# Optimization experiments

Hardware: AMD Instinct MI355X
Metric: run time of the kernel (lower is better)

The kernel has to match this reference:

```python
import jax, jax.numpy as jnp
import numpy as np

N, E, D, H, G = 50000, 1_600_000, 13, 32, 128
EPS = 1e-5


def _lin(k, fan_in, fan_out):
    kw, kb = jax.random.split(k)
    bound = 1.0 / np.sqrt(fan_in)
    W = jax.random.uniform(kw, (fan_in, fan_out), jnp.float32, -bound, bound)
    b = jax.random.uniform(kb, (fan_out,), jnp.float32, -bound, bound)
    return W, b


def setup_inputs() -> dict:
    key = jax.random.key(0)
    ks = jax.random.split(key, 10)
    x = jax.random.normal(ks[0], (N, D), jnp.float32)
    edge_index = jax.random.randint(ks[1], (2, E), 0, N)
    batch = jnp.sort(jax.random.randint(ks[2], (N,), 0, G))
    bn_gamma = jnp.ones((D,), jnp.float32)
    bn_beta = jnp.zeros((D,), jnp.float32)
    in_w1, in_b1 = _lin(ks[3], D, H)
    in_w2, in_b2 = _lin(ks[4], H, H)
    conv_w1, conv_b1 = _lin(ks[5], 2 * (H + D), 2 * H)
    conv_w2, conv_b2 = _lin(ks[6], 2 * H, H)
    out_w1, out_b1 = _lin(ks[7], H + D, H)
    out_w2, out_b2 = _lin(ks[8], H, 1)
    return dict(x=x, edge_index=edge_index, batch=batch,
                bn_gamma=bn_gamma, bn_beta=bn_beta,
                in_w1=in_w1, in_b1=in_b1, in_w2=in_w2, in_b2=in_b2,
                conv_w1=conv_w1, conv_b1=conv_b1, conv_w2=conv_w2, conv_b2=conv_b2,
                out_w1=out_w1, out_b1=out_b1, out_w2=out_w2, out_b2=out_b2)


def reference(x, edge_index, batch, bn_gamma, bn_beta,
              in_w1, in_b1, in_w2, in_b2,
              conv_w1, conv_b1, conv_w2, conv_b2,
              out_w1, out_b1, out_w2, out_b2):
    # BatchNorm1d (training-mode batch statistics, biased variance)
    mu = jnp.mean(x, axis=0)
    var = jnp.mean((x - mu) ** 2, axis=0)
    X = (x - mu) / jnp.sqrt(var + EPS) * bn_gamma + bn_beta  # [N, D]
    # inputnet
    Hn = jnp.tanh(jax.nn.relu(X @ in_w1 + in_b1) @ in_w2 + in_b2)  # [N, H]
    feat = jnp.concatenate([Hn, X], axis=-1)  # [N, H+D]
    # n_iters = 1 EdgeConv iteration: message = nn([x_i, x_j - x_i]), aggr='add' at target i
    src, dst = edge_index[0], edge_index[1]
    x_i = feat[dst]                               # [E, H+D] target
    x_j = feat[src]                               # [E, H+D] source
    m = jnp.concatenate([x_i, x_j - x_i], axis=-1)  # [E, 2(H+D)]
    m = jnp.tanh(jax.nn.relu(m @ conv_w1 + conv_b1) @ conv_w2 + conv_b2)  # [E, H]
    Hn = jax.ops.segment_sum(m, dst, num_segments=N)  # [N, H]
    feat = jnp.concatenate([Hn, X], axis=-1)  # [N, H+D]
    # global_mean_pool over graphs
    sums = jax.ops.segment_sum(feat, batch, num_segments=G)  # [G, H+D]
    counts = jax.ops.segment_sum(jnp.ones((feat.shape[0], 1), feat.dtype), batch, num_segments=G)
    x_mean = sums / jnp.maximum(counts, 1.0)
    # outputnet
    return jax.nn.sigmoid(jax.nn.relu(x_mean @ out_w1 + out_b1) @ out_w2 + out_b2)  # [G, 1]
```

## Files before the change

### kernel.cpp

```cpp
#include <hip/hip_runtime.h>


typedef __attribute__((ext_vector_type(4))) float floatx4;
typedef __attribute__((ext_vector_type(8))) short short8;
typedef __attribute__((ext_vector_type(8))) _Float16 half8;
typedef __attribute__((ext_vector_type(2))) __fp16 fp16x2;

__device__ __forceinline__ unsigned short f2bf(float f) {
    unsigned int u = __float_as_uint(f);
    u += 0x7FFFu + ((u >> 16) & 1u);
    return (unsigned short)(u >> 16);
}
__device__ __forceinline__ unsigned short f2h(float f) {
    _Float16 h = (_Float16)f;
    return __builtin_bit_cast(unsigned short, h);
}
__device__ __forceinline__ float h2f(unsigned short u) {
    return (float)__builtin_bit_cast(_Float16, u);
}
__device__ __forceinline__ float fast_tanh(float x) {
    float ax = fminf(fabsf(x), 20.0f);
    float e = __expf(2.0f * ax);
    float r = 1.0f - 2.0f * __builtin_amdgcn_rcpf(e + 1.0f);
    return copysignf(r, x);
}
__device__ __forceinline__ float fast_sigmoid(float x) {
    float xc = fminf(fmaxf(x, -30.f), 30.f);
    return 1.0f / (1.0f + __expf(-xc));
}
__device__ __forceinline__ unsigned int pk_h2(float a, float b) {
    fp16x2 p = __builtin_amdgcn_cvt_pkrtz(a, b);
    return __builtin_bit_cast(unsigned int, p);
}
__device__ __forceinline__ void atomic_pk_add_f16(unsigned short* addr, unsigned int packed) {
    asm volatile("global_atomic_pk_add_f16 %0, %1, off" :: "v"(addr), "v"(packed) : "memory");
}

#define NBLK_STAT 120

__global__ __launch_bounds__(256) void k_bnstat(const float* __restrict__ x, int N,
                                                float* __restrict__ part,
                                                uint4* __restrict__ HnZ, int hnq,
                                                float* __restrict__ gacc, int gn,
                                                const float* __restrict__ conv_w1,
                                                unsigned short* __restrict__ wcat) {
    int tid = blockIdx.x * blockDim.x + threadIdx.x;
    int stride = gridDim.x * blockDim.x;
    uint4 z4 = make_uint4(0u, 0u, 0u, 0u);
    for (int i = tid; i < hnq; i += stride) HnZ[i] = z4;
    for (int i = tid; i < gn; i += stride) gacc[i] = 0.f;
    for (int i = tid; i < 128 * 64; i += stride) {
        int c = i >> 6, k = i & 63;
        float v = 0.f;
        if (k < 45) {
            int cc = c & 63;
            float bot = conv_w1[(45 + k) * 64 + cc];
            v = (c < 64) ? (conv_w1[k * 64 + cc] - bot) : bot;
        }
        wcat[i] = f2bf(v);
    }

    float s[13], q[13];
#pragma unroll
    for (int d = 0; d < 13; d++) { s[d] = 0.f; q[d] = 0.f; }
    for (int n = tid; n < N; n += stride) {
        const float* row = x + (size_t)n * 13;
#pragma unroll
        for (int d = 0; d < 13; d++) { float f = row[d]; s[d] += f; q[d] += f * f; }
    }
#pragma unroll
    for (int d = 0; d < 13; d++) {
        for (int off = 32; off > 0; off >>= 1) {
            s[d] += __shfl_down(s[d], off, 64);
            q[d] += __shfl_down(q[d], off, 64);
        }
    }
    __shared__ float red[4][26];
    int w = threadIdx.x >> 6;
    if ((threadIdx.x & 63) == 0) {
#pragma unroll
        for (int d = 0; d < 13; d++) { red[w][d] = s[d]; red[w][13 + d] = q[d]; }
    }
    __syncthreads();
    if (threadIdx.x < 26) {
        float v = red[0][threadIdx.x] + red[1][threadIdx.x] + red[2][threadIdx.x] + red[3][threadIdx.x];
        int d = threadIdx.x;
        if (d < 13) part[blockIdx.x * 32 + d] = v;
        else        part[NBLK_STAT * 32 + blockIdx.x * 32 + (d - 13)] = v;
    }
}

__global__ __launch_bounds__(256) void k_nodeA(
    const float* __restrict__ x, const int* __restrict__ batch,
    const float* __restrict__ bn_g, const float* __restrict__ bn_b,
    const float* __restrict__ in_w1, const float* __restrict__ in_b1,
    const float* __restrict__ in_w2, const float* __restrict__ in_b2,
    const float* __restrict__ part,
    unsigned short* __restrict__ feat, float* __restrict__ gacc, int N) {
    __shared__ float sW1[13 * 32], sB1[32], sW2[32 * 32], sB2[32];
    __shared__ float sScl[16], sShf[16];
    __shared__ float sRedS[13][8], sRedQ[13][8];
    __shared__ unsigned short sFeat[256 * 64];
    int tid = threadIdx.x;

    for (int i = tid; i < 13 * 32; i += 256) sW1[i] = in_w1[i];
    if (tid < 32) { sB1[tid] = in_b1[tid]; sB2[tid] = in_b2[tid]; }
    for (int i = tid; i < 32 * 32; i += 256) sW2[i] = in_w2[i];
    if (tid < 104) {
        int d = tid >> 3, j = tid & 7;
        float su = 0.f, sq = 0.f;
        for (int b = j; b < NBLK_STAT; b += 8) {
            su += part[b * 32 + d];
            sq += part[NBLK_STAT * 32 + b * 32 + d];
        }
        sRedS[d][j] = su; sRedQ[d][j] = sq;
    }
    __syncthreads();
    if (tid < 13) {
        float su = 0.f, sq = 0.f;
#pragma unroll
        for (int j = 0; j < 8; j++) { su += sRedS[tid][j]; sq += sRedQ[tid][j]; }
        float invN = 1.0f / (float)N;
        float mu = su * invN;
        float var = fmaxf(sq * invN - mu * mu, 0.f);
        float sc = bn_g[tid] / sqrtf(var + 1e-5f);
        sScl[tid] = sc;
        sShf[tid] = bn_b[tid] - mu * sc;
    }
    __syncthreads();

    int n = blockIdx.x * 256 + tid;
    bool valid = (n < N);
    int nl = valid ? n : (N - 1);

    float X[13];
#pragma unroll
    for (int d = 0; d < 13; d++)
        X[d] = x[(size_t)nl * 13 + d] * sScl[d] + sShf[d];
    float h1[32];
#pragma unroll
    for (int j = 0; j < 32; j++) {
        float acc = sB1[j];
#pragma unroll
        for (int d = 0; d < 13; d++) acc += X[d] * sW1[d * 32 + j];
        h1[j] = fmaxf(acc, 0.f);
    }
    float h2[32];
#pragma unroll
    for (int j = 0; j < 32; j++) {
        float acc = sB2[j];
#pragma unroll
        for (int k = 0; k < 32; k++) acc += h1[k] * sW2[k * 32 + j];
        h2[j] = fast_tanh(acc);
    }

    unsigned int fw[16];
#pragma unroll
    for (int i = 0; i < 16; i++) fw[i] = 0;
    unsigned int xw[7];
#pragma unroll
    for (int i = 0; i < 7; i++) xw[i] = 0;
    if (valid) {
#pragma unroll
        for (int i = 0; i < 16; i++)
            fw[i] = (unsigned)f2bf(h2[2 * i]) | ((unsigned)f2bf(h2[2 * i + 1]) << 16);
#pragma unroll
        for (int i = 0; i < 6; i++)
            xw[i] = (unsigned)f2bf(X[2 * i]) | ((unsigned)f2bf(X[2 * i + 1]) << 16);
        xw[6] = (unsigned)f2bf(X[12]);
    }
    {
        unsigned short* row = sFeat + tid * 64;
        ((uint4*)row)[0] = make_uint4(fw[0], fw[1], fw[2], fw[3]);
        ((uint4*)row)[1] = make_uint4(fw[4], fw[5], fw[6], fw[7]);
        ((uint4*)row)[2] = make_uint4(fw[8], fw[9], fw[10], fw[11]);
        ((uint4*)row)[3] = make_uint4(fw[12], fw[13], fw[14], fw[15]);
        ((uint4*)row)[4] = make_uint4(xw[0], xw[1], xw[2], xw[3]);
        ((uint4*)row)[5] = make_uint4(xw[4], xw[5], xw[6], 0u);
        ((uint4*)row)[6] = make_uint4(0u, 0u, 0u, 0u);
        ((uint4*)row)[7] = make_uint4(0u, 0u, 0u, 0u);
    }

    {
        int g = valid ? batch[n] : -1;
        unsigned long long uni = __ballot(g == __shfl(g, 0, 64));
        if (uni == ~0ull && g >= 0) {
            float red[14];
#pragma unroll
            for (int d = 0; d < 13; d++) red[d] = X[d];
            red[13] = 1.0f;
#pragma unroll
            for (int d = 0; d < 14; d++)
                for (int off = 32; off > 0; off >>= 1)
                    red[d] += __shfl_down(red[d], off, 64);
            if ((tid & 63) == 0) {
#pragma unroll
                for (int d = 0; d < 13; d++) unsafeAtomicAdd(&gacc[g * 46 + 32 + d], red[d]);
                unsafeAtomicAdd(&gacc[g * 46 + 45], red[13]);
            }
        } else if (valid) {
#pragma unroll
            for (int d = 0; d < 13; d++) unsafeAtomicAdd(&gacc[g * 46 + 32 + d], X[d]);
            unsafeAtomicAdd(&gacc[g * 46 + 45], 1.0f);
        }
    }
    __syncthreads();

    uint4* dst = (uint4*)(feat + (size_t)blockIdx.x * 256 * 64);
    const uint4* srcq = (const uint4*)sFeat;
#pragma unroll
    for (int j = 0; j < 8; j++) dst[tid + j * 256] = srcq[tid + j * 256];
}

__global__ __launch_bounds__(256) void k_nodeB(
    const unsigned short* __restrict__ feat, const unsigned short* __restrict__ wcat,
    const float* __restrict__ conv_b1,
    unsigned short* __restrict__ A, unsigned short* __restrict__ Bm, int N) {
    int tid = threadIdx.x;
    int lane = tid & 63;
    int w = tid >> 6;
    int q = lane >> 4;
    int m = lane & 15;

    short8 wf[2][8];
#pragma unroll
    for (int ks = 0; ks < 2; ks++)
#pragma unroll
        for (int t = 0; t < 8; t++)
            wf[ks][t] = *(const short8*)(wcat + (t * 16 + m) * 64 + ks * 32 + q * 8);
    float cb1v[4];
#pragma unroll
    for (int t = 0; t < 4; t++) cb1v[t] = conv_b1[t * 16 + m];

    int row0 = blockIdx.x * 64 + w * 16;
    const unsigned short* ar = feat + (size_t)(row0 + m) * 64;
    short8 a0 = *(const short8*)(ar + q * 8);
    short8 a1 = *(const short8*)(ar + 32 + q * 8);
    floatx4 c[8];
#pragma unroll
    for (int t = 0; t < 8; t++) {
        floatx4 z = {0.f, 0.f, 0.f, 0.f};
        c[t] = __builtin_amdgcn_mfma_f32_16x16x32_bf16(a0, wf[0][t], z, 0, 0, 0);
        c[t] = __builtin_amdgcn_mfma_f32_16x16x32_bf16(a1, wf[1][t], c[t], 0, 0, 0);
    }
#pragma unroll
    for (int r = 0; r < 4; r++) {
        int row = row0 + (q << 2) + r;
        if (row < N) {
#pragma unroll
            for (int t = 0; t < 4; t++)
                A[(size_t)row * 64 + t * 16 + m] = f2h(c[t][r] + cb1v[t]);
#pragma unroll
            for (int t = 4; t < 8; t++)
                Bm[(size_t)row * 64 + (t - 4) * 16 + m] = f2h(c[t][r]);
        }
    }
}

__global__ __launch_bounds__(256) void k_edge(
    const int* __restrict__ ei,
    const unsigned short* __restrict__ A, const unsigned short* __restrict__ Bm,
    const float* __restrict__ conv_w2, const float* __restrict__ conv_b2,
    unsigned short* __restrict__ Hn, int E) {
    int lane = threadIdx.x & 63;
    int wid  = blockIdx.x * (blockDim.x >> 6) + (threadIdx.x >> 6);
    int nw   = gridDim.x * (blockDim.x >> 6);
    int q = lane >> 4;
    int m = lane & 15;

    half8 wf[2][2];
#pragma unroll
    for (int s = 0; s < 2; s++)
#pragma unroll
        for (int t = 0; t < 2; t++)
#pragma unroll
            for (int j = 0; j < 8; j++)
                wf[s][t][j] = (_Float16)conv_w2[(s * 32 + q * 8 + j) * 32 + 2 * m + t];
    float cb2a = conv_b2[2 * m];
    float cb2b = conv_b2[2 * m + 1];

    const int* srcp = ei;
    const int* dstp = ei + E;
    int npairs = E >> 5;

    const half8 zero8 = (half8)(_Float16)0.0f;

    for (int p = wid; p < npairs; p += nw) {
        int e0 = p << 5;
        int vd0 = dstp[e0 + m];
        int vs0 = srcp[e0 + m];
        int vd1 = dstp[e0 + 16 + m];
        int vs1 = srcp[e0 + 16 + m];
        uint4 av0a = *(const uint4*)(A  + (size_t)vd0 * 64 + q * 8);
        uint4 av0b = *(const uint4*)(A  + (size_t)vd0 * 64 + 32 + q * 8);
        uint4 bv0a = *(const uint4*)(Bm + (size_t)vs0 * 64 + q * 8);
        uint4 bv0b = *(const uint4*)(Bm + (size_t)vs0 * 64 + 32 + q * 8);
        uint4 av1a = *(const uint4*)(A  + (size_t)vd1 * 64 + q * 8);
        uint4 av1b = *(const uint4*)(A  + (size_t)vd1 * 64 + 32 + q * 8);
        uint4 bv1a = *(const uint4*)(Bm + (size_t)vs1 * 64 + q * 8);
        uint4 bv1b = *(const uint4*)(Bm + (size_t)vs1 * 64 + 32 + q * 8);

        auto mk = [&zero8](uint4 av, uint4 bv) -> half8 {
            half8 a = __builtin_bit_cast(half8, av);
            half8 b = __builtin_bit_cast(half8, bv);
            half8 s = a + b;
            return __builtin_elementwise_max(s, zero8);
        };
        half8 h0a = mk(av0a, bv0a);
        half8 h0b = mk(av0b, bv0b);
        half8 h1a = mk(av1a, bv1a);
        half8 h1b = mk(av1b, bv1b);

        floatx4 c00 = {0.f, 0.f, 0.f, 0.f}, c01 = {0.f, 0.f, 0.f, 0.f};
        floatx4 c10 = {0.f, 0.f, 0.f, 0.f}, c11 = {0.f, 0.f, 0.f, 0.f};
        c00 = __builtin_amdgcn_mfma_f32_16x16x32_f16(h0a, wf[0][0], c00, 0, 0, 0);
        c01 = __builtin_amdgcn_mfma_f32_16x16x32_f16(h0a, wf[0][1], c01, 0, 0, 0);
        c10 = __builtin_amdgcn_mfma_f32_16x16x32_f16(h1a, wf[0][0], c10, 0, 0, 0);
        c11 = __builtin_amdgcn_mfma_f32_16x16x32_f16(h1a, wf[0][1], c11, 0, 0, 0);
        c00 = __builtin_amdgcn_mfma_f32_16x16x32_f16(h0b, wf[1][0], c00, 0, 0, 0);
        c01 = __builtin_amdgcn_mfma_f32_16x16x32_f16(h0b, wf[1][1], c01, 0, 0, 0);
        c10 = __builtin_amdgcn_mfma_f32_16x16x32_f16(h1b, wf[1][0], c10, 0, 0, 0);
        c11 = __builtin_amdgcn_mfma_f32_16x16x32_f16(h1b, wf[1][1], c11, 0, 0, 0);

#pragma unroll
        for (int r = 0; r < 4; r++) {
            int m2 = (q << 2) + r;
            int dd0 = __shfl(vd0, m2, 64);
            int dd1 = __shfl(vd1, m2, 64);
            float o00 = fast_tanh(c00[r] + cb2a);
            float o01 = fast_tanh(c01[r] + cb2b);
            float o10 = fast_tanh(c10[r] + cb2a);
            float o11 = fast_tanh(c11[r] + cb2b);
            atomic_pk_add_f16(Hn + (size_t)dd0 * 32 + 2 * m, pk_h2(o00, o01));
            atomic_pk_add_f16(Hn + (size_t)dd1 * 32 + 2 * m, pk_h2(o10, o11));
        }
    }

    int tstart = npairs << 5;
    int tail = E - tstart;
    if (tail && wid == 0 && lane < tail) {
        int e = tstart + lane;
        int vd = dstp[e], vs = srcp[e];
        float h[64];
        for (int k = 0; k < 64; k++) {
            float a = h2f(A[(size_t)vd * 64 + k]);
            float b = h2f(Bm[(size_t)vs * 64 + k]);
            h[k] = fmaxf(a + b, 0.f);
        }
        for (int j = 0; j < 16; j++) {
            float acc0 = conv_b2[2 * j], acc1 = conv_b2[2 * j + 1];
            for (int k = 0; k < 64; k++) {
                acc0 += h[k] * conv_w2[k * 32 + 2 * j];
                acc1 += h[k] * conv_w2[k * 32 + 2 * j + 1];
            }
            atomic_pk_add_f16(Hn + (size_t)vd * 32 + 2 * j, pk_h2(fast_tanh(acc0), fast_tanh(acc1)));
        }
    }
}

__global__ __launch_bounds__(256) void k_pool(const unsigned short* __restrict__ Hn,
                                              const int* __restrict__ batch,
                                              float* __restrict__ gacc, int N) {
    const int NPB = 128;
    int c = threadIdx.x & 31;
    int r = threadIdx.x >> 5;
    int n0 = blockIdx.x * NPB;
    int nend = min(n0 + NPB, N);
    int gcur = -1;
    float acc = 0.f;
    for (int n = n0 + r; n < nend; n += 8) {
        int g = batch[n];
        if (g != gcur) {
            if (gcur >= 0) unsafeAtomicAdd(&gacc[gcur * 46 + c], acc);
            gcur = g; acc = 0.f;
        }
        acc += h2f(Hn[(size_t)n * 32 + c]);
    }
    if (gcur >= 0) unsafeAtomicAdd(&gacc[gcur * 46 + c], acc);
}

__global__ void k_out(const float* __restrict__ gacc,
                      const float* __restrict__ out_w1, const float* __restrict__ out_b1,
                      const float* __restrict__ out_w2, const float* __restrict__ out_b2,
                      float* __restrict__ out, int G) {
    int g = blockIdx.x * blockDim.x + threadIdx.x;
    if (g >= G) return;
    float cnt = fmaxf(gacc[g * 46 + 45], 1.0f);
    float inv = 1.0f / cnt;
    float f[45];
#pragma unroll
    for (int i = 0; i < 45; i++) f[i] = gacc[g * 46 + i] * inv;
    float h[32];
#pragma unroll
    for (int j = 0; j < 32; j++) {
        float acc = out_b1[j];
#pragma unroll
        for (int k = 0; k < 45; k++) acc += f[k] * out_w1[k * 32 + j];
        h[j] = fmaxf(acc, 0.f);
    }
    float o = out_b2[0];
#pragma unroll
    for (int j = 0; j < 32; j++) o += h[j] * out_w2[j];
    out[g] = fast_sigmoid(o);
}

extern "C" void kernel_launch(void* const* d_in, const int* in_sizes, int n_in,
                              void* d_out, int out_size, void* d_ws, size_t ws_size,
                              hipStream_t stream) {
    const float* x      = (const float*)d_in[0];
    const int*   ei     = (const int*)d_in[1];
    const int*   batch  = (const int*)d_in[2];
    const float* bn_g   = (const float*)d_in[3];
    const float* bn_b   = (const float*)d_in[4];
    const float* in_w1  = (const float*)d_in[5];
    const float* in_b1  = (const float*)d_in[6];
    const float* in_w2  = (const float*)d_in[7];
    const float* in_b2  = (const float*)d_in[8];
    const float* cw1    = (const float*)d_in[9];
    const float* cb1    = (const float*)d_in[10];
    const float* cw2    = (const float*)d_in[11];
    const float* cb2    = (const float*)d_in[12];
    const float* ow1    = (const float*)d_in[13];
    const float* ob1    = (const float*)d_in[14];
    const float* ow2    = (const float*)d_in[15];
    const float* ob2    = (const float*)d_in[16];

    int N = in_sizes[0] / 13;
    int E = in_sizes[1] / 2;
    int G = out_size;
    int Npad = (N + 255) & ~255;

    auto al = [](size_t v) { return (v + 255) & ~(size_t)255; };
    char* ws = (char*)d_ws;
    size_t hn_off   = 0;
    size_t gacc_off = al((size_t)N * 32 * 2);
    size_t part_off = gacc_off + al((size_t)G * 46 * 4);
    size_t a_off    = part_off + al(2 * NBLK_STAT * 32 * 4);
    size_t b_off    = a_off + al((size_t)Npad * 64 * 2);
    size_t ft_off   = b_off + al((size_t)Npad * 64 * 2);
    size_t wc_off   = ft_off + al((size_t)Npad * 64 * 2);

    unsigned short* Hn   = (unsigned short*)(ws + hn_off);
    float* gacc          = (float*)(ws + gacc_off);
    float* part          = (float*)(ws + part_off);
    unsigned short* A    = (unsigned short*)(ws + a_off);
    unsigned short* Bm   = (unsigned short*)(ws + b_off);
    unsigned short* feat = (unsigned short*)(ws + ft_off);
    unsigned short* wcat = (unsigned short*)(ws + wc_off);

    int hnq = (N * 32 * 2) / 16;
    int gn  = G * 46;

    k_bnstat<<<NBLK_STAT, 256, 0, stream>>>(x, N, part, (uint4*)Hn, hnq, gacc, gn,
                                            cw1, wcat);
    k_nodeA<<<Npad / 256, 256, 0, stream>>>(x, batch, bn_g, bn_b,
                                            in_w1, in_b1, in_w2, in_b2,
                                            part, feat, gacc, N);
    k_nodeB<<<Npad / 64, 256, 0, stream>>>(feat, wcat, cb1, A, Bm, N);
    k_edge<<<2048, 256, 0, stream>>>(ei, A, Bm, cw2, cb2, Hn, E);
    k_pool<<<(N + 127) / 128, 256, 0, stream>>>(Hn, batch, gacc, N);
    k_out<<<1, 128, 0, stream>>>(gacc, ow1, ob1, ow2, ob2, (float*)d_out, G);
}
```

Before: 261.2 us.

## Fuse edge messages directly into per-graph pooling via shared-memory accumulators

Since per-node Hn is only used after summing over graphs, edge messages are accumulated straight into per-graph sums, looked up through batch[dst]. This is done with shared-memory float atomics per block, then flushed to global. It removes the N×32 Hn buffer, its zeroing, the global fp16 packed atomics and the separate pooling kernel. In exchange it adds a per-edge batch lookup, heavy LDS atomic contention on few graph rows, a 16KB shared buffer per block, and it assumes G ≤ 128.

```diff
diff --git a/kernel.cpp b/kernel.cpp
--- a/kernel.cpp
+++ b/kernel.cpp
@@ -28,26 +28,17 @@
     float xc = fminf(fmaxf(x, -30.f), 30.f);
     return 1.0f / (1.0f + __expf(-xc));
 }
-__device__ __forceinline__ unsigned int pk_h2(float a, float b) {
-    fp16x2 p = __builtin_amdgcn_cvt_pkrtz(a, b);
-    return __builtin_bit_cast(unsigned int, p);
-}
-__device__ __forceinline__ void atomic_pk_add_f16(unsigned short* addr, unsigned int packed) {
-    asm volatile("global_atomic_pk_add_f16 %0, %1, off" :: "v"(addr), "v"(packed) : "memory");
-}
 
 #define NBLK_STAT 120
+#define GMAX 128
 
 __global__ __launch_bounds__(256) void k_bnstat(const float* __restrict__ x, int N,
                                                 float* __restrict__ part,
-                                                uint4* __restrict__ HnZ, int hnq,
                                                 float* __restrict__ gacc, int gn,
                                                 const float* __restrict__ conv_w1,
                                                 unsigned short* __restrict__ wcat) {
     int tid = blockIdx.x * blockDim.x + threadIdx.x;
     int stride = gridDim.x * blockDim.x;
-    uint4 z4 = make_uint4(0u, 0u, 0u, 0u);
-    for (int i = tid; i < hnq; i += stride) HnZ[i] = z4;
     for (int i = tid; i < gn; i += stride) gacc[i] = 0.f;
     for (int i = tid; i < 128 * 64; i += stride) {
         int c = i >> 6, k = i & 63;
@@ -257,13 +248,18 @@
     }
 }
 
-__global__ __launch_bounds__(256) void k_edge(
+__global__ __launch_bounds__(256) void k_edgeg(
     const int* __restrict__ ei,
     const unsigned short* __restrict__ A, const unsigned short* __restrict__ Bm,
     const float* __restrict__ conv_w2, const float* __restrict__ conv_b2,
-    unsigned short* __restrict__ Hn, int E) {
-    int lane = threadIdx.x & 63;
-    int wid  = blockIdx.x * (blockDim.x >> 6) + (threadIdx.x >> 6);
+    const int* __restrict__ batch,
+    float* __restrict__ gacc, int E) {
+    __shared__ float sAcc[GMAX][32];
+    int tid = threadIdx.x;
+    for (int i = tid; i < GMAX * 32; i += 256) ((float*)sAcc)[i] = 0.f;
+
+    int lane = tid & 63;
+    int wid  = blockIdx.x * (blockDim.x >> 6) + (tid >> 6);
     int nw   = gridDim.x * (blockDim.x >> 6);
     int q = lane >> 4;
     int m = lane & 15;
@@ -284,6 +280,8 @@
     int npairs = E >> 5;
 
     const half8 zero8 = (half8)(_Float16)0.0f;
+
+    __syncthreads();
 
     for (int p = wid; p < npairs; p += nw) {
         int e0 = p << 5;
@@ -291,6 +289,8 @@
         int vs0 = srcp[e0 + m];
         int vd1 = dstp[e0 + 16 + m];
         int vs1 = srcp[e0 + 16 + m];
+        int gd0 = batch[vd0];
+        int gd1 = batch[vd1];
         uint4 av0a = *(const uint4*)(A  + (size_t)vd0 * 64 + q * 8);
         uint4 av0b = *(const uint4*)(A  + (size_t)vd0 * 64 + 32 + q * 8);
         uint4 bv0a = *(const uint4*)(Bm + (size_t)vs0 * 64 + q * 8);
@@ -325,58 +325,44 @@
 #pragma unroll
         for (int r = 0; r < 4; r++) {
             int m2 = (q << 2) + r;
-            int dd0 = __shfl(vd0, m2, 64);
-            int dd1 = __shfl(vd1, m2, 64);
+            int gg0 = __shfl(gd0, m2, 64);
+            int gg1 = __shfl(gd1, m2, 64);
             float o00 = fast_tanh(c00[r] + cb2a);
             float o01 = fast_tanh(c01[r] + cb2b);
             float o10 = fast_tanh(c10[r] + cb2a);
             float o11 = fast_tanh(c11[r] + cb2b);
-            atomic_pk_add_f16(Hn + (size_t)dd0 * 32 + 2 * m, pk_h2(o00, o01));
-            atomic_pk_add_f16(Hn + (size_t)dd1 * 32 + 2 * m, pk_h2(o10, o11));
+            atomicAdd(&sAcc[gg0][2 * m], o00);
+            atomicAdd(&sAcc[gg0][2 * m + 1], o01);
+            atomicAdd(&sAcc[gg1][2 * m], o10);
+            atomicAdd(&sAcc[gg1][2 * m + 1], o11);
         }
     }
 
     int tstart = npairs << 5;
     int tail = E - tstart;
-    if (tail && wid == 0 && lane < tail) {
-        int e = tstart + lane;
+    if (tail && blockIdx.x == 0 && tid < tail) {
+        int e = tstart + tid;
         int vd = dstp[e], vs = srcp[e];
+        int g = batch[vd];
         float h[64];
         for (int k = 0; k < 64; k++) {
             float a = h2f(A[(size_t)vd * 64 + k]);
             float b = h2f(Bm[(size_t)vs * 64 + k]);
             h[k] = fmaxf(a + b, 0.f);
         }
-        for (int j = 0; j < 16; j++) {
-            float acc0 = conv_b2[2 * j], acc1 = conv_b2[2 * j + 1];
-            for (int k = 0; k < 64; k++) {
-                acc0 += h[k] * conv_w2[k * 32 + 2 * j];
-                acc1 += h[k] * conv_w2[k * 32 + 2 * j + 1];
-            }
-            atomic_pk_add_f16(Hn + (size_t)vd * 32 + 2 * j, pk_h2(fast_tanh(acc0), fast_tanh(acc1)));
-        }
-    }
-}
-
-__global__ __launch_bounds__(256) void k_pool(const unsigned short* __restrict__ Hn,
-                                              const int* __restrict__ batch,
-                                              float* __restrict__ gacc, int N) {
-    const int NPB = 128;
-    int c = threadIdx.x & 31;
-    int r = threadIdx.x >> 5;
-    int n0 = blockIdx.x * NPB;
-    int nend = min(n0 + NPB, N);
-    int gcur = -1;
-    float acc = 0.f;
-    for (int n = n0 + r; n < nend; n += 8) {
-        int g = batch[n];
-        if (g != gcur) {
-            if (gcur >= 0) unsafeAtomicAdd(&gacc[gcur * 46 + c], acc);
-            gcur = g; acc = 0.f;
-        }
-        acc += h2f(Hn[(size_t)n * 32 + c]);
-    }
-    if (gcur >= 0) unsafeAtomicAdd(&gacc[gcur * 46 + c], acc);
+        for (int j = 0; j < 32; j++) {
+            float acc = conv_b2[j];
+            for (int k = 0; k < 64; k++) acc += h[k] * conv_w2[k * 32 + j];
+            atomicAdd(&sAcc[g][j], fast_tanh(acc));
+        }
+    }
+
+    __syncthreads();
+    for (int i = tid; i < GMAX * 32; i += 256) {
+        int g = i >> 5, c = i & 31;
+        float v = sAcc[g][c];
+        if (v != 0.f) unsafeAtomicAdd(&gacc[g * 46 + c], v);
+    }
 }
 
 __global__ void k_out(const float* __restrict__ gacc,
@@ -432,15 +418,13 @@
 
     auto al = [](size_t v) { return (v + 255) & ~(size_t)255; };
     char* ws = (char*)d_ws;
-    size_t hn_off   = 0;
-    size_t gacc_off = al((size_t)N * 32 * 2);
+    size_t gacc_off = 0;
     size_t part_off = gacc_off + al((size_t)G * 46 * 4);
     size_t a_off    = part_off + al(2 * NBLK_STAT * 32 * 4);
     size_t b_off    = a_off + al((size_t)Npad * 64 * 2);
     size_t ft_off   = b_off + al((size_t)Npad * 64 * 2);
     size_t wc_off   = ft_off + al((size_t)Npad * 64 * 2);
 
-    unsigned short* Hn   = (unsigned short*)(ws + hn_off);
     float* gacc          = (float*)(ws + gacc_off);
     float* part          = (float*)(ws + part_off);
     unsigned short* A    = (unsigned short*)(ws + a_off);
@@ -448,16 +432,13 @@
     unsigned short* feat = (unsigned short*)(ws + ft_off);
     unsigned short* wcat = (unsigned short*)(ws + wc_off);
 
-    int hnq = (N * 32 * 2) / 16;
-    int gn  = G * 46;
-
-    k_bnstat<<<NBLK_STAT, 256, 0, stream>>>(x, N, part, (uint4*)Hn, hnq, gacc, gn,
-                                            cw1, wcat);
+    int gn = G * 46;
+
+    k_bnstat<<<NBLK_STAT, 256, 0, stream>>>(x, N, part, gacc, gn, cw1, wcat);
     k_nodeA<<<Npad / 256, 256, 0, stream>>>(x, batch, bn_g, bn_b,
                                             in_w1, in_b1, in_w2, in_b2,
                                             part, feat, gacc, N);
     k_nodeB<<<Npad / 64, 256, 0, stream>>>(feat, wcat, cb1, A, Bm, N);
-    k_edge<<<2048, 256, 0, stream>>>(ei, A, Bm, cw2, cb2, Hn, E);
-    k_pool<<<(N + 127) / 128, 256, 0, stream>>>(Hn, batch, gacc, N);
+    k_edgeg<<<2048, 256, 0, stream>>>(ei, A, Bm, cw2, cb2, batch, gacc, E);
     k_out<<<1, 128, 0, stream>>>(gacc, ow1, ob1, ow2, ob2, (float*)d_out, G);
 }
```

Measured after the change: 428.3 us. 64.0% more time.
